# Kernel optimization log

Hardware: AMD Instinct MI355X
Metric: run time of the kernel (lower is better)

The kernel has to match this reference:

```python
import jax, jax.numpy as jnp
import numpy as np

VOCAB = 50000
DIM = 128
B = 1024
LQ = 32
LD = 512
KERNEL_NUM = 21
SIGMA = 0.1
EXACT_SIGMA = 0.001
OUT_LAYERS = [10, 5]
EPS = 1e-12  # F.normalize eps


def _kernel_params():
    step = 2.0 / (KERNEL_NUM - 1)
    mus = (np.arange(-1.0, 1.0, step) + step / 2).astype(np.float32)  # 20 soft bins
    mus = np.concatenate([mus, np.array([1.0], dtype=np.float32)])   # exact-match bin
    sigmas = np.array([SIGMA] * (KERNEL_NUM - 1) + [EXACT_SIGMA], dtype=np.float32)
    return mus, sigmas


def _normalize(x):
    n = jnp.linalg.norm(x, axis=-1, keepdims=True)
    return x / jnp.maximum(n, EPS)


def _predict(emb, w0, b0, w1, b1, w2, b2, q, d):
    eq = _normalize(emb[q])  # [B, Lq, D]
    ed = _normalize(emb[d])  # [B, Ld, D]
    mm = jnp.einsum('bld,brd->blr', eq, ed)  # cosine matching matrix [B, Lq, Ld]
    mus, sigmas = _kernel_params()
    feats = [
        jnp.log1p(jnp.exp(-(mm - mu) ** 2 / (2.0 * sig * sig)).sum(-1)).sum(-1)
        for mu, sig in zip(mus, sigmas)
    ]
    x = jnp.stack(feats, axis=1)  # [B, KERNEL_NUM]
    h = jax.nn.relu(x @ w0.T + b0)
    h = jax.nn.relu(h @ w1.T + b1)
    return h @ w2.T + b2  # [B, 1]


def setup_inputs() -> dict:
    key = jax.random.key(0)
    ks = jax.random.split(key, 12)
    emb = jax.random.normal(ks[0], (VOCAB, DIM), jnp.float32) * 0.1
    emb = emb.at[0].set(0.0)  # padding_idx=0 row
    q1 = jax.random.randint(ks[1], (B, LQ), 0, VOCAB)
    d1 = jax.random.randint(ks[2], (B, LD), 0, VOCAB)
    q2 = jax.random.randint(ks[3], (B, LQ), 0, VOCAB)
    d2 = jax.random.randint(ks[4], (B, LD), 0, VOCAB)
    dims = [KERNEL_NUM] + OUT_LAYERS + [1]
    def lin(k, fan_in, fan_out):
        bound = 1.0 / np.sqrt(fan_in)
        kw, kb = jax.random.split(k)
        w = jax.random.uniform(kw, (fan_out, fan_in), jnp.float32, -bound, bound)
        b = jax.random.uniform(kb, (fan_out,), jnp.float32, -bound, bound)
        return w, b
    w0, b0 = lin(ks[5], dims[0], dims[1])
    w1, b1 = lin(ks[6], dims[1], dims[2])
    w2, b2 = lin(ks[7], dims[2], dims[3])
    return dict(emb=emb, w0=w0, b0=b0, w1=w1, b1=b1, w2=w2, b2=b2,
                query_1=q1, document_1=d1, query_2=q2, document_2=d2)


def reference(emb, w0, b0, w1, b1, w2, b2, query_1, document_1, query_2, document_2):
    logits_1 = _predict(emb, w0, b0, w1, b1, w2, b2, query_1, document_1)
    logits_2 = _predict(emb, w0, b0, w1, b1, w2, b2, query_2, document_2)
    return jax.nn.sigmoid(logits_1 - logits_2)
```

## Files before the change

kernel.cpp:

```cpp
#include <hip/hip_runtime.h>
#include <hip/hip_bf16.h>
#include <math.h>

#define LQ    32
#define LD    512
#define DIM   128
#define NK    21
#define VOCAB 50000

typedef __attribute__((ext_vector_type(8))) short short8;
typedef __attribute__((ext_vector_type(4))) float f32x4;
typedef __attribute__((ext_vector_type(2))) float f32x2;

__device__ __forceinline__ unsigned pkbf(float a, float b) {
    unsigned short ua = __bfloat16_as_ushort(__float2bfloat16(a));
    unsigned short ub = __bfloat16_as_ushort(__float2bfloat16(b));
    return (unsigned)ua | ((unsigned)ub << 16);
}

__global__ __launch_bounds__(256, 8)
void knrm_prep(const float* __restrict__ emb, unsigned* __restrict__ emb16) {
    int row  = blockIdx.x * 4 + (threadIdx.x >> 6);
    int lane = threadIdx.x & 63;
    if (row >= VOCAB) return;
    float2 v = ((const float2*)(emb + (size_t)row * DIM))[lane];
    float ss = v.x * v.x + v.y * v.y;
    #pragma unroll
    for (int s = 1; s < 64; s <<= 1) ss += __shfl_xor(ss, s, 64);
    float rn = 1.0f / fmaxf(sqrtf(ss), 1e-12f);
    emb16[(size_t)row * 64 + lane] = pkbf(v.x * rn, v.y * rn);
}

__global__ __launch_bounds__(256, 4)
void knrm_main(const unsigned short* __restrict__ emb16,
               const float* __restrict__ w0, const float* __restrict__ b0,
               const float* __restrict__ w1, const float* __restrict__ b1,
               const float* __restrict__ w2, const float* __restrict__ b2,
               const int* __restrict__ q1, const int* __restrict__ d1,
               const int* __restrict__ q2, const int* __restrict__ d2,
               float* __restrict__ logits)
{
    __shared__ __align__(16) char smem[16320];
    unsigned short (*Bq)[DIM] = (unsigned short(*)[DIM])(smem);
    float (*SSh)[LQ][20] = (float(*)[LQ][20])(smem);
    int*   dtokS = (int*)(smem + 10240);
    float (*SSe)[LQ] = (float(*)[LQ])(smem + 12288);
    int*   qtokS = (int*)(smem + 13312);
    float* Lbuf  = (float*)(smem + 13440);
    float* xk    = (float*)(smem + 16128);
    float* h0s   = (float*)(smem + 16224);
    float* h1s   = (float*)(smem + 16264);

    const int bid  = blockIdx.x;
    const int b    = bid >> 1;
    const int side = bid & 1;
    const int tid  = threadIdx.x;
    const int w    = tid >> 6;
    const int lane = tid & 63;
    const int rg   = lane >> 4;
    const int l15  = lane & 15;

    const int* qt = (side ? q2 : q1) + b * LQ;
    const int* dt = (side ? d2 : d1) + b * LD;

    if (tid < LQ) qtokS[tid] = qt[tid];
    dtokS[tid]       = dt[tid];
    dtokS[tid + 256] = dt[tid + 256];
    __syncthreads();

    {
        #pragma unroll
        for (int cc = 0; cc < 2; ++cc) {
            int rloc = cc * 4 + rg;
            int tok  = qtokS[w * 8 + rloc];
            int sw   = (rloc & 7) << 3;
            int col  = (l15 * 8) ^ sw;
            const unsigned short* src = emb16 + (size_t)tok * DIM + col;
            __builtin_amdgcn_global_load_lds(src, &Bq[w * 8 + cc * 4][0], 16, 0, 0);
        }
    }

    {
        int q = tid & 31, g = tid >> 5;
        int qv = qtokS[q];
        int c = 0;
        const int4* dp = (const int4*)&dtokS[g * 64];
        #pragma unroll
        for (int j = 0; j < 16; ++j) {
            int4 dv = dp[j];
            c += (dv.x == qv) + (dv.y == qv) + (dv.z == qv) + (dv.w == qv);
        }
        SSe[g][q] = (qv == 0) ? 0.0f : (float)c;
    }
    __syncthreads();

    const int dbase = w * 128;
    int tok0 = dtokS[dbase + l15];
    const unsigned short* ap0 = emb16 + (size_t)tok0 * DIM + rg * 8;
    short8 a0 = *(const short8*)(ap0);
    short8 a1 = *(const short8*)(ap0 + 32);
    short8 a2 = *(const short8*)(ap0 + 64);
    short8 a3 = *(const short8*)(ap0 + 96);

    const int swB = (l15 & 7) << 3;
    short8 bq0[4], bq1[4];
    #pragma unroll
    for (int g = 0; g < 4; ++g) {
        bq0[g] = *(const short8*)&Bq[l15][(g * 32 + rg * 8) ^ swB];
        bq1[g] = *(const short8*)&Bq[l15 + 16][(g * 32 + rg * 8) ^ swB];
    }
    __syncthreads();

    f32x2 accP[10], accM[10];
    #pragma unroll
    for (int j = 0; j < 10; ++j) {
        accP[j] = (f32x2){0.0f, 0.0f};
        accM[j] = (f32x2){0.0f, 0.0f};
    }

    auto chain2 = [&](f32x2 x, f32x2* AP, f32x2* AM) {
        f32x2 t1 = x * -72.134752f + 7.2134752f;
        f32x2 Ea = t1 * x + -0.18033688f;
        f32x2 Ra = x * 14.4269504f + -0.7213475f;
        f32x2 E, R, rc;
        E.x = __builtin_amdgcn_exp2f(Ea.x);
        E.y = __builtin_amdgcn_exp2f(Ea.y);
        R.x = __builtin_amdgcn_exp2f(Ra.x);
        R.y = __builtin_amdgcn_exp2f(Ra.y);
        rc.x = __builtin_amdgcn_rcpf(R.x);
        rc.y = __builtin_amdgcn_rcpf(R.y);
        f32x2 tP = E;
        f32x2 tM = E * rc;
        AP[0] += tP; AM[0] += tM;
        #pragma unroll
        for (int j = 1; j < 10; ++j) {
            tP *= R; tM *= rc;
            AP[j] += tP; AM[j] += tM;
        }
    };

    #pragma unroll 1
    for (int t = 0; t < 8; ++t) {
        f32x4 c0 = {0, 0, 0, 0}, c1 = {0, 0, 0, 0};
        c0 = __builtin_amdgcn_mfma_f32_16x16x32_bf16(a0, bq0[0], c0, 0, 0, 0);
        c1 = __builtin_amdgcn_mfma_f32_16x16x32_bf16(a0, bq1[0], c1, 0, 0, 0);
        c0 = __builtin_amdgcn_mfma_f32_16x16x32_bf16(a1, bq0[1], c0, 0, 0, 0);
        c1 = __builtin_amdgcn_mfma_f32_16x16x32_bf16(a1, bq1[1], c1, 0, 0, 0);
        c0 = __builtin_amdgcn_mfma_f32_16x16x32_bf16(a2, bq0[2], c0, 0, 0, 0);
        c1 = __builtin_amdgcn_mfma_f32_16x16x32_bf16(a2, bq1[2], c1, 0, 0, 0);
        c0 = __builtin_amdgcn_mfma_f32_16x16x32_bf16(a3, bq0[3], c0, 0, 0, 0);
        c1 = __builtin_amdgcn_mfma_f32_16x16x32_bf16(a3, bq1[3], c1, 0, 0, 0);

        int nt = (t < 7) ? (t + 1) : 7;
        int ntok = dtokS[dbase + nt * 16 + l15];
        const unsigned short* np = emb16 + (size_t)ntok * DIM + rg * 8;
        short8 n0 = *(const short8*)(np);
        short8 n1 = *(const short8*)(np + 32);
        short8 n2 = *(const short8*)(np + 64);
        short8 n3 = *(const short8*)(np + 96);

        #pragma unroll
        for (int r = 0; r < 4; ++r) {
            f32x2 x;
            x.x = c0[r];
            x.y = c1[r];
            chain2(x, accP, accM);
        }

        a0 = n0; a1 = n1; a2 = n2; a3 = n3;
    }

    #pragma unroll
    for (int j = 0; j < 10; ++j) {
        accP[j].x += __shfl_xor(accP[j].x, 16, 64); accP[j].x += __shfl_xor(accP[j].x, 32, 64);
        accP[j].y += __shfl_xor(accP[j].y, 16, 64); accP[j].y += __shfl_xor(accP[j].y, 32, 64);
        accM[j].x += __shfl_xor(accM[j].x, 16, 64); accM[j].x += __shfl_xor(accM[j].x, 32, 64);
        accM[j].y += __shfl_xor(accM[j].y, 16, 64); accM[j].y += __shfl_xor(accM[j].y, 32, 64);
    }
    if (lane < 16) {
        const float GP[10] = {1.0f, 0.60653066f, 0.13533528f, 0.011108997f,
                              3.3546263e-4f, 3.7266532e-6f, 1.5229979e-8f,
                              2.2897348e-11f, 1.2664166e-14f, 2.5767430e-18f};
        const float GM[10] = {0.60653066f, 0.13533528f, 0.011108997f,
                              3.3546263e-4f, 3.7266532e-6f, 1.5229979e-8f,
                              2.2897348e-11f, 1.2664166e-14f, 2.5767430e-18f,
                              1.9287498e-22f};
        #pragma unroll
        for (int j = 0; j < 10; ++j) {
            SSh[w][l15][10 + j]      = accP[j].x * GP[j];
            SSh[w][l15][9 - j]       = accM[j].x * GM[j];
            SSh[w][l15 + 16][10 + j] = accP[j].y * GP[j];
            SSh[w][l15 + 16][9 - j]  = accM[j].y * GM[j];
        }
    }
    __syncthreads();

    for (int idx = tid; idx < LQ * NK; idx += 256) {
        int q = idx / NK, k = idx - q * NK;
        float s;
        if (k == 20) {
            s = SSe[0][q] + SSe[1][q] + SSe[2][q] + SSe[3][q]
              + SSe[4][q] + SSe[5][q] + SSe[6][q] + SSe[7][q];
        } else {
            s = SSh[0][q][k] + SSh[1][q][k] + SSh[2][q][k] + SSh[3][q][k];
        }
        Lbuf[idx] = log1pf(s);
    }
    __syncthreads();

    if (tid < NK) {
        float s = 0.0f;
        #pragma unroll 1
        for (int q = 0; q < LQ; ++q) s += Lbuf[q * NK + tid];
        xk[tid] = s;
    }
    __syncthreads();

    if (tid < 10) {
        float s = b0[tid];
        #pragma unroll
        for (int k = 0; k < NK; ++k) s = fmaf(xk[k], w0[tid * NK + k], s);
        h0s[tid] = fmaxf(s, 0.0f);
    }
    __syncthreads();
    if (tid < 5) {
        float s = b1[tid];
        #pragma unroll
        for (int k = 0; k < 10; ++k) s = fmaf(h0s[k], w1[tid * 10 + k], s);
        h1s[tid] = fmaxf(s, 0.0f);
    }
    __syncthreads();
    if (tid == 0) {
        float s = b2[0];
        #pragma unroll
        for (int k = 0; k < 5; ++k) s = fmaf(h1s[k], w2[k], s);
        logits[bid] = s;
    }
}

__global__ void knrm_fin(const float* __restrict__ lg, float* __restrict__ out) {
    int i = blockIdx.x * 256 + threadIdx.x;
    if (i < 1024) {
        float z = lg[2 * i] - lg[2 * i + 1];
        out[i] = 1.0f / (1.0f + __expf(-z));
    }
}

extern "C" void kernel_launch(void* const* d_in, const int* in_sizes, int n_in,
                              void* d_out, int out_size, void* d_ws, size_t ws_size,
                              hipStream_t stream) {
    const float* emb = (const float*)d_in[0];
    const float* w0  = (const float*)d_in[1];
    const float* b0  = (const float*)d_in[2];
    const float* w1  = (const float*)d_in[3];
    const float* b1  = (const float*)d_in[4];
    const float* w2  = (const float*)d_in[5];
    const float* b2  = (const float*)d_in[6];
    const int*   q1  = (const int*)d_in[7];
    const int*   d1  = (const int*)d_in[8];
    const int*   q2  = (const int*)d_in[9];
    const int*   d2  = (const int*)d_in[10];
    float* out = (float*)d_out;

    unsigned* emb16 = (unsigned*)d_ws;
    float* logits   = (float*)((char*)d_ws + 12800000);

    knrm_prep<<<(VOCAB + 3) / 4, 256, 0, stream>>>(emb, emb16);
    knrm_main<<<2048, 256, 0, stream>>>((const unsigned short*)emb16,
                                        w0, b0, w1, b1, w2, b2,
                                        q1, d1, q2, d2, logits);
    knrm_fin<<<4, 256, 0, stream>>>(logits, out);
}
```

Baseline: 65.91 us.

## Process both query/document pairs per block and fuse sigmoid into main kernel

Each block now handles both sides of a batch element in a loop, halving the grid to 1024 blocks and computing the final sigmoid in-kernel, which removes the separate finalize launch. It also peels the last MFMA iteration to avoid a redundant prefetch and reduces the log1p/query sum in parallel per wave instead of a serial 21-thread loop. The trade-off is less parallelism across blocks and serialized sides within a block, which may lower occupancy-driven latency hiding.

```diff
diff --git a/kernel.cpp b/kernel.cpp
--- a/kernel.cpp
+++ b/kernel.cpp
@@ -38,211 +38,221 @@
                const float* __restrict__ w2, const float* __restrict__ b2,
                const int* __restrict__ q1, const int* __restrict__ d1,
                const int* __restrict__ q2, const int* __restrict__ d2,
-               float* __restrict__ logits)
+               float* __restrict__ out)
 {
-    __shared__ __align__(16) char smem[16320];
+    __shared__ __align__(16) char smem[16016];
     unsigned short (*Bq)[DIM] = (unsigned short(*)[DIM])(smem);
     float (*SSh)[LQ][20] = (float(*)[LQ][20])(smem);
-    int*   dtokS = (int*)(smem + 10240);
+    int*   dtok0 = (int*)(smem + 10240);
     float (*SSe)[LQ] = (float(*)[LQ])(smem + 12288);
-    int*   qtokS = (int*)(smem + 13312);
-    float* Lbuf  = (float*)(smem + 13440);
-    float* xk    = (float*)(smem + 16128);
-    float* h0s   = (float*)(smem + 16224);
-    float* h1s   = (float*)(smem + 16264);
-
-    const int bid  = blockIdx.x;
-    const int b    = bid >> 1;
-    const int side = bid & 1;
+    int*   qtok0 = (int*)(smem + 13312);
+    float* xw    = (float*)(smem + 13440);
+    float* h0s   = (float*)(smem + 13776);
+    float* h1s   = (float*)(smem + 13816);
+    int*   dtok1 = (int*)(smem + 13840);
+    int*   qtok1 = (int*)(smem + 15888);
+
+    const int b    = blockIdx.x;
     const int tid  = threadIdx.x;
     const int w    = tid >> 6;
     const int lane = tid & 63;
     const int rg   = lane >> 4;
     const int l15  = lane & 15;
 
-    const int* qt = (side ? q2 : q1) + b * LQ;
-    const int* dt = (side ? d2 : d1) + b * LD;
-
-    if (tid < LQ) qtokS[tid] = qt[tid];
-    dtokS[tid]       = dt[tid];
-    dtokS[tid + 256] = dt[tid + 256];
+    if (tid < LQ) {
+        qtok0[tid] = q1[b * LQ + tid];
+        qtok1[tid] = q2[b * LQ + tid];
+    }
+    dtok0[tid]       = d1[b * LD + tid];
+    dtok0[tid + 256] = d1[b * LD + tid + 256];
+    dtok1[tid]       = d2[b * LD + tid];
+    dtok1[tid + 256] = d2[b * LD + tid + 256];
     __syncthreads();
 
-    {
+    float lg0 = 0.0f;
+
+    #pragma unroll 1
+    for (int side = 0; side < 2; ++side) {
+        const int* qts = side ? qtok1 : qtok0;
+        const int* dts = side ? dtok1 : dtok0;
+
         #pragma unroll
         for (int cc = 0; cc < 2; ++cc) {
             int rloc = cc * 4 + rg;
-            int tok  = qtokS[w * 8 + rloc];
+            int tok  = qts[w * 8 + rloc];
             int sw   = (rloc & 7) << 3;
             int col  = (l15 * 8) ^ sw;
             const unsigned short* src = emb16 + (size_t)tok * DIM + col;
             __builtin_amdgcn_global_load_lds(src, &Bq[w * 8 + cc * 4][0], 16, 0, 0);
         }
-    }
-
-    {
-        int q = tid & 31, g = tid >> 5;
-        int qv = qtokS[q];
-        int c = 0;
-        const int4* dp = (const int4*)&dtokS[g * 64];
-        #pragma unroll
-        for (int j = 0; j < 16; ++j) {
-            int4 dv = dp[j];
-            c += (dv.x == qv) + (dv.y == qv) + (dv.z == qv) + (dv.w == qv);
-        }
-        SSe[g][q] = (qv == 0) ? 0.0f : (float)c;
-    }
-    __syncthreads();
-
-    const int dbase = w * 128;
-    int tok0 = dtokS[dbase + l15];
-    const unsigned short* ap0 = emb16 + (size_t)tok0 * DIM + rg * 8;
-    short8 a0 = *(const short8*)(ap0);
-    short8 a1 = *(const short8*)(ap0 + 32);
-    short8 a2 = *(const short8*)(ap0 + 64);
-    short8 a3 = *(const short8*)(ap0 + 96);
-
-    const int swB = (l15 & 7) << 3;
-    short8 bq0[4], bq1[4];
-    #pragma unroll
-    for (int g = 0; g < 4; ++g) {
-        bq0[g] = *(const short8*)&Bq[l15][(g * 32 + rg * 8) ^ swB];
-        bq1[g] = *(const short8*)&Bq[l15 + 16][(g * 32 + rg * 8) ^ swB];
-    }
-    __syncthreads();
-
-    f32x2 accP[10], accM[10];
-    #pragma unroll
-    for (int j = 0; j < 10; ++j) {
-        accP[j] = (f32x2){0.0f, 0.0f};
-        accM[j] = (f32x2){0.0f, 0.0f};
-    }
-
-    auto chain2 = [&](f32x2 x, f32x2* AP, f32x2* AM) {
-        f32x2 t1 = x * -72.134752f + 7.2134752f;
-        f32x2 Ea = t1 * x + -0.18033688f;
-        f32x2 Ra = x * 14.4269504f + -0.7213475f;
-        f32x2 E, R, rc;
-        E.x = __builtin_amdgcn_exp2f(Ea.x);
-        E.y = __builtin_amdgcn_exp2f(Ea.y);
-        R.x = __builtin_amdgcn_exp2f(Ra.x);
-        R.y = __builtin_amdgcn_exp2f(Ra.y);
-        rc.x = __builtin_amdgcn_rcpf(R.x);
-        rc.y = __builtin_amdgcn_rcpf(R.y);
-        f32x2 tP = E;
-        f32x2 tM = E * rc;
-        AP[0] += tP; AM[0] += tM;
-        #pragma unroll
-        for (int j = 1; j < 10; ++j) {
-            tP *= R; tM *= rc;
-            AP[j] += tP; AM[j] += tM;
-        }
-    };
-
-    #pragma unroll 1
-    for (int t = 0; t < 8; ++t) {
-        f32x4 c0 = {0, 0, 0, 0}, c1 = {0, 0, 0, 0};
-        c0 = __builtin_amdgcn_mfma_f32_16x16x32_bf16(a0, bq0[0], c0, 0, 0, 0);
-        c1 = __builtin_amdgcn_mfma_f32_16x16x32_bf16(a0, bq1[0], c1, 0, 0, 0);
-        c0 = __builtin_amdgcn_mfma_f32_16x16x32_bf16(a1, bq0[1], c0, 0, 0, 0);
-        c1 = __builtin_amdgcn_mfma_f32_16x16x32_bf16(a1, bq1[1], c1, 0, 0, 0);
-        c0 = __builtin_amdgcn_mfma_f32_16x16x32_bf16(a2, bq0[2], c0, 0, 0, 0);
-        c1 = __builtin_amdgcn_mfma_f32_16x16x32_bf16(a2, bq1[2], c1, 0, 0, 0);
-        c0 = __builtin_amdgcn_mfma_f32_16x16x32_bf16(a3, bq0[3], c0, 0, 0, 0);
-        c1 = __builtin_amdgcn_mfma_f32_16x16x32_bf16(a3, bq1[3], c1, 0, 0, 0);
-
-        int nt = (t < 7) ? (t + 1) : 7;
-        int ntok = dtokS[dbase + nt * 16 + l15];
-        const unsigned short* np = emb16 + (size_t)ntok * DIM + rg * 8;
-        short8 n0 = *(const short8*)(np);
-        short8 n1 = *(const short8*)(np + 32);
-        short8 n2 = *(const short8*)(np + 64);
-        short8 n3 = *(const short8*)(np + 96);
-
-        #pragma unroll
-        for (int r = 0; r < 4; ++r) {
-            f32x2 x;
-            x.x = c0[r];
-            x.y = c1[r];
-            chain2(x, accP, accM);
-        }
-
-        a0 = n0; a1 = n1; a2 = n2; a3 = n3;
-    }
-
-    #pragma unroll
-    for (int j = 0; j < 10; ++j) {
-        accP[j].x += __shfl_xor(accP[j].x, 16, 64); accP[j].x += __shfl_xor(accP[j].x, 32, 64);
-        accP[j].y += __shfl_xor(accP[j].y, 16, 64); accP[j].y += __shfl_xor(accP[j].y, 32, 64);
-        accM[j].x += __shfl_xor(accM[j].x, 16, 64); accM[j].x += __shfl_xor(accM[j].x, 32, 64);
-        accM[j].y += __shfl_xor(accM[j].y, 16, 64); accM[j].y += __shfl_xor(accM[j].y, 32, 64);
-    }
-    if (lane < 16) {
-        const float GP[10] = {1.0f, 0.60653066f, 0.13533528f, 0.011108997f,
-                              3.3546263e-4f, 3.7266532e-6f, 1.5229979e-8f,
-                              2.2897348e-11f, 1.2664166e-14f, 2.5767430e-18f};
-        const float GM[10] = {0.60653066f, 0.13533528f, 0.011108997f,
-                              3.3546263e-4f, 3.7266532e-6f, 1.5229979e-8f,
-                              2.2897348e-11f, 1.2664166e-14f, 2.5767430e-18f,
-                              1.9287498e-22f};
+
+        {
+            int q = tid & 31, g = tid >> 5;
+            int qv = qts[q];
+            int c = 0;
+            const int4* dp = (const int4*)&dts[g * 64];
+            #pragma unroll
+            for (int j = 0; j < 16; ++j) {
+                int4 dv = dp[j];
+                c += (dv.x == qv) + (dv.y == qv) + (dv.z == qv) + (dv.w == qv);
+            }
+            SSe[g][q] = (qv == 0) ? 0.0f : (float)c;
+        }
+        __syncthreads();
+
+        const int dbase = w * 128;
+        int tok0 = dts[dbase + l15];
+        const unsigned short* ap0 = emb16 + (size_t)tok0 * DIM + rg * 8;
+        short8 a0 = *(const short8*)(ap0);
+        short8 a1 = *(const short8*)(ap0 + 32);
+        short8 a2 = *(const short8*)(ap0 + 64);
+        short8 a3 = *(const short8*)(ap0 + 96);
+
+        const int swB = (l15 & 7) << 3;
+        short8 bq0[4], bq1[4];
+        #pragma unroll
+        for (int g = 0; g < 4; ++g) {
+            bq0[g] = *(const short8*)&Bq[l15][(g * 32 + rg * 8) ^ swB];
+            bq1[g] = *(const short8*)&Bq[l15 + 16][(g * 32 + rg * 8) ^ swB];
+        }
+        __syncthreads();
+
+        f32x2 accP[10], accM[10];
         #pragma unroll
         for (int j = 0; j < 10; ++j) {
-            SSh[w][l15][10 + j]      = accP[j].x * GP[j];
-            SSh[w][l15][9 - j]       = accM[j].x * GM[j];
-            SSh[w][l15 + 16][10 + j] = accP[j].y * GP[j];
-            SSh[w][l15 + 16][9 - j]  = accM[j].y * GM[j];
-        }
-    }
-    __syncthreads();
-
-    for (int idx = tid; idx < LQ * NK; idx += 256) {
-        int q = idx / NK, k = idx - q * NK;
-        float s;
-        if (k == 20) {
-            s = SSe[0][q] + SSe[1][q] + SSe[2][q] + SSe[3][q]
-              + SSe[4][q] + SSe[5][q] + SSe[6][q] + SSe[7][q];
-        } else {
-            s = SSh[0][q][k] + SSh[1][q][k] + SSh[2][q][k] + SSh[3][q][k];
-        }
-        Lbuf[idx] = log1pf(s);
-    }
-    __syncthreads();
-
-    if (tid < NK) {
-        float s = 0.0f;
+            accP[j] = (f32x2){0.0f, 0.0f};
+            accM[j] = (f32x2){0.0f, 0.0f};
+        }
+
+        auto chain2 = [&](f32x2 x) {
+            f32x2 t1 = x * -72.134752f + 7.2134752f;
+            f32x2 Ea = t1 * x + -0.18033688f;
+            f32x2 Ra = x * 14.4269504f + -0.7213475f;
+            f32x2 E, R, rc;
+            E.x = __builtin_amdgcn_exp2f(Ea.x);
+            E.y = __builtin_amdgcn_exp2f(Ea.y);
+            R.x = __builtin_amdgcn_exp2f(Ra.x);
+            R.y = __builtin_amdgcn_exp2f(Ra.y);
+            rc.x = __builtin_amdgcn_rcpf(R.x);
+            rc.y = __builtin_amdgcn_rcpf(R.y);
+            f32x2 tP = E;
+            f32x2 tM = E * rc;
+            accP[0] += tP; accM[0] += tM;
+            #pragma unroll
+            for (int j = 1; j < 10; ++j) {
+                tP *= R; tM *= rc;
+                accP[j] += tP; accM[j] += tM;
+            }
+        };
+
+        auto mfma8 = [&](f32x4& c0, f32x4& c1) {
+            c0 = __builtin_amdgcn_mfma_f32_16x16x32_bf16(a0, bq0[0], c0, 0, 0, 0);
+            c1 = __builtin_amdgcn_mfma_f32_16x16x32_bf16(a0, bq1[0], c1, 0, 0, 0);
+            c0 = __builtin_amdgcn_mfma_f32_16x16x32_bf16(a1, bq0[1], c0, 0, 0, 0);
+            c1 = __builtin_amdgcn_mfma_f32_16x16x32_bf16(a1, bq1[1], c1, 0, 0, 0);
+            c0 = __builtin_amdgcn_mfma_f32_16x16x32_bf16(a2, bq0[2], c0, 0, 0, 0);
+            c1 = __builtin_amdgcn_mfma_f32_16x16x32_bf16(a2, bq1[2], c1, 0, 0, 0);
+            c0 = __builtin_amdgcn_mfma_f32_16x16x32_bf16(a3, bq0[3], c0, 0, 0, 0);
+            c1 = __builtin_amdgcn_mfma_f32_16x16x32_bf16(a3, bq1[3], c1, 0, 0, 0);
+        };
+
         #pragma unroll 1
-        for (int q = 0; q < LQ; ++q) s += Lbuf[q * NK + tid];
-        xk[tid] = s;
-    }
-    __syncthreads();
-
-    if (tid < 10) {
-        float s = b0[tid];
-        #pragma unroll
-        for (int k = 0; k < NK; ++k) s = fmaf(xk[k], w0[tid * NK + k], s);
-        h0s[tid] = fmaxf(s, 0.0f);
-    }
-    __syncthreads();
-    if (tid < 5) {
-        float s = b1[tid];
-        #pragma unroll
-        for (int k = 0; k < 10; ++k) s = fmaf(h0s[k], w1[tid * 10 + k], s);
-        h1s[tid] = fmaxf(s, 0.0f);
-    }
-    __syncthreads();
-    if (tid == 0) {
-        float s = b2[0];
-        #pragma unroll
-        for (int k = 0; k < 5; ++k) s = fmaf(h1s[k], w2[k], s);
-        logits[bid] = s;
-    }
-}
-
-__global__ void knrm_fin(const float* __restrict__ lg, float* __restrict__ out) {
-    int i = blockIdx.x * 256 + threadIdx.x;
-    if (i < 1024) {
-        float z = lg[2 * i] - lg[2 * i + 1];
-        out[i] = 1.0f / (1.0f + __expf(-z));
+        for (int t = 0; t < 7; ++t) {
+            f32x4 c0 = {0, 0, 0, 0}, c1 = {0, 0, 0, 0};
+            mfma8(c0, c1);
+
+            int ntok = dts[dbase + (t + 1) * 16 + l15];
+            const unsigned short* np = emb16 + (size_t)ntok * DIM + rg * 8;
+            short8 n0 = *(const short8*)(np);
+            short8 n1 = *(const short8*)(np + 32);
+            short8 n2 = *(const short8*)(np + 64);
+            short8 n3 = *(const short8*)(np + 96);
+
+            #pragma unroll
+            for (int r = 0; r < 4; ++r) {
+                f32x2 x; x.x = c0[r]; x.y = c1[r];
+                chain2(x);
+            }
+            a0 = n0; a1 = n1; a2 = n2; a3 = n3;
+        }
+        {
+            f32x4 c0 = {0, 0, 0, 0}, c1 = {0, 0, 0, 0};
+            mfma8(c0, c1);
+            #pragma unroll
+            for (int r = 0; r < 4; ++r) {
+                f32x2 x; x.x = c0[r]; x.y = c1[r];
+                chain2(x);
+            }
+        }
+
+        #pragma unroll
+        for (int j = 0; j < 10; ++j) {
+            accP[j].x += __shfl_xor(accP[j].x, 16, 64); accP[j].x += __shfl_xor(accP[j].x, 32, 64);
+            accP[j].y += __shfl_xor(accP[j].y, 16, 64); accP[j].y += __shfl_xor(accP[j].y, 32, 64);
+            accM[j].x += __shfl_xor(accM[j].x, 16, 64); accM[j].x += __shfl_xor(accM[j].x, 32, 64);
+            accM[j].y += __shfl_xor(accM[j].y, 16, 64); accM[j].y += __shfl_xor(accM[j].y, 32, 64);
+        }
+        if (lane < 16) {
+            const float GP[10] = {1.0f, 0.60653066f, 0.13533528f, 0.011108997f,
+                                  3.3546263e-4f, 3.7266532e-6f, 1.5229979e-8f,
+                                  2.2897348e-11f, 1.2664166e-14f, 2.5767430e-18f};
+            const float GM[10] = {0.60653066f, 0.13533528f, 0.011108997f,
+                                  3.3546263e-4f, 3.7266532e-6f, 1.5229979e-8f,
+                                  2.2897348e-11f, 1.2664166e-14f, 2.5767430e-18f,
+                                  1.9287498e-22f};
+            #pragma unroll
+            for (int j = 0; j < 10; ++j) {
+                SSh[w][l15][10 + j]      = accP[j].x * GP[j];
+                SSh[w][l15][9 - j]       = accM[j].x * GM[j];
+                SSh[w][l15 + 16][10 + j] = accP[j].y * GP[j];
+                SSh[w][l15 + 16][9 - j]  = accM[j].y * GM[j];
+            }
+        }
+        __syncthreads();
+
+        if (lane < NK) {
+            float s = 0.0f;
+            #pragma unroll
+            for (int qq = 0; qq < 8; ++qq) {
+                int q = w * 8 + qq;
+                float v;
+                if (lane == 20) {
+                    v = SSe[0][q] + SSe[1][q] + SSe[2][q] + SSe[3][q]
+                      + SSe[4][q] + SSe[5][q] + SSe[6][q] + SSe[7][q];
+                } else {
+                    v = SSh[0][q][lane] + SSh[1][q][lane]
+                      + SSh[2][q][lane] + SSh[3][q][lane];
+                }
+                s += log1pf(v);
+            }
+            xw[w * NK + lane] = s;
+        }
+        __syncthreads();
+
+        if (tid < 10) {
+            float s = b0[tid];
+            #pragma unroll
+            for (int k = 0; k < NK; ++k) {
+                float xv = xw[k] + xw[NK + k] + xw[2 * NK + k] + xw[3 * NK + k];
+                s = fmaf(xv, w0[tid * NK + k], s);
+            }
+            h0s[tid] = fmaxf(s, 0.0f);
+        }
+        __syncthreads();
+        if (tid < 5) {
+            float s = b1[tid];
+            #pragma unroll
+            for (int k = 0; k < 10; ++k) s = fmaf(h0s[k], w1[tid * 10 + k], s);
+            h1s[tid] = fmaxf(s, 0.0f);
+        }
+        __syncthreads();
+        if (tid == 0) {
+            float s = b2[0];
+            #pragma unroll
+            for (int k = 0; k < 5; ++k) s = fmaf(h1s[k], w2[k], s);
+            if (side == 0) lg0 = s;
+            else out[b] = 1.0f / (1.0f + __expf(-(lg0 - s)));
+        }
     }
 }
 
@@ -263,11 +273,9 @@
     float* out = (float*)d_out;
 
     unsigned* emb16 = (unsigned*)d_ws;
-    float* logits   = (float*)((char*)d_ws + 12800000);
 
     knrm_prep<<<(VOCAB + 3) / 4, 256, 0, stream>>>(emb, emb16);
-    knrm_main<<<2048, 256, 0, stream>>>((const unsigned short*)emb16,
+    knrm_main<<<1024, 256, 0, stream>>>((const unsigned short*)emb16,
                                         w0, b0, w1, b1, w2, b2,
-                                        q1, d1, q2, d2, logits);
-    knrm_fin<<<4, 256, 0, stream>>>(logits, out);
-}
+                                        q1, d1, q2, d2, out);
+}
```

Measured after the change: 82.07 us. 24.5% more time.
